# Performance work log

Measured on AMD Instinct MI355X. Metric: run time of the kernel, lower is better.

The kernel has to match this reference:

```python
import jax, jax.numpy as jnp
import numpy as np

B, S, D_MODEL, H = 2, 2048, 2048, 16
DQK = D_MODEL // H            # 128
DV = D_MODEL * 2 // H // 3    # 85 (GLU branch)
SCALE = DQK ** -0.5
ROPE_BASE = 10000.0


def apply_rope(x):
    # x: [B, S, H, D], NeoX-style half rotation
    D = x.shape[-1]
    half = D // 2
    inv_freq = 1.0 / (ROPE_BASE ** (jnp.arange(half, dtype=jnp.float32) / half))
    ang = jnp.arange(x.shape[1], dtype=jnp.float32)[:, None] * inv_freq[None, :]  # [S, half]
    cos = jnp.cos(ang)[None, :, None, :]
    sin = jnp.sin(ang)[None, :, None, :]
    x1, x2 = x[..., :half], x[..., half:]
    return jnp.concatenate([x1 * cos - x2 * sin, x2 * cos + x1 * sin], axis=-1)


def setup_inputs() -> dict:
    key = jax.random.key(0)
    ks = jax.random.split(key, 12)
    init = lambda k, shape, fan_in: jax.random.uniform(k, shape, jnp.float32, -1.0, 1.0) * (fan_in ** -0.5)
    q = jax.random.normal(ks[0], (B, S, D_MODEL), jnp.float32)
    k = jax.random.normal(ks[1], (B, S, D_MODEL), jnp.float32)
    v = jax.random.normal(ks[2], (B, S, D_MODEL), jnp.float32)
    # causal boolean mask: True = masked (upper triangle)
    mask = jnp.triu(jnp.ones((S, S), dtype=bool), k=1)
    Wq = init(ks[3], (D_MODEL, DQK * H), D_MODEL)
    bq = init(ks[4], (DQK * H,), D_MODEL)
    Wk = init(ks[5], (D_MODEL, DQK * H), D_MODEL)
    bk = init(ks[6], (DQK * H,), D_MODEL)
    Wv = init(ks[7], (D_MODEL, DV * H * 2), D_MODEL)
    bv = init(ks[8], (DV * H * 2,), D_MODEL)
    Wo = init(ks[9], (DV * H, D_MODEL), DV * H)
    bo = init(ks[10], (D_MODEL,), DV * H)
    return {"q": q, "k": k, "v": v, "mask": mask,
            "Wq": Wq, "bq": bq, "Wk": Wk, "bk": bk,
            "Wv": Wv, "bv": bv, "Wo": Wo, "bo": bo}


def reference(q, k, v, mask, Wq, bq, Wk, bk, Wv, bv, Wo, bo):
    qp = q @ Wq + bq                      # [B,S,H*DQK]
    kp = k @ Wk + bk                      # [B,S,H*DQK]
    vp = v @ Wv + bv                      # [B,S,2*H*DV]
    # GLU over the FULL last dim (matches torch chunk(2, dim=-1) before unflatten)
    half = DV * H
    vg = vp[..., :half] * jax.nn.silu(vp[..., half:])   # [B,S,H*DV]
    qh = qp.reshape(B, S, H, DQK)
    kh = kp.reshape(B, S, H, DQK)
    vh = vg.reshape(B, S, H, DV)
    qh = apply_rope(qh)
    kh = apply_rope(kh)
    # [B,H,S,D]
    qh = qh.transpose(0, 2, 1, 3)
    kh = kh.transpose(0, 2, 1, 3)
    vh = vh.transpose(0, 2, 1, 3)
    score = jnp.einsum('bhqd,bhkd->bhqk', qh, kh) * SCALE  # [B,H,S,S]
    score = jnp.where(mask[None, None, :, :], -jnp.inf, score)
    attn = jax.nn.softmax(score, axis=-1)
    o = jnp.einsum('bhqk,bhkd->bhqd', attn, vh)            # [B,H,S,DV]
    o = o.transpose(0, 2, 1, 3).reshape(B, S, H * DV)
    return o @ Wo + bo                                     # [B,S,D_MODEL]
```

## Files before the change

kernel.cpp:

```cpp
#include <hip/hip_runtime.h>
#include <cstdint>
#include <cmath>

typedef __bf16 bf16;
typedef __bf16 bf16x8 __attribute__((ext_vector_type(8)));
typedef float f32x4 __attribute__((ext_vector_type(4)));

#define B_      2
#define S_      2048
#define H_      16
#define DQK_    128
#define DV_     85
#define DVP_    96
#define DMODEL_ 2048
#define NKV_    1360
#define KH_     1536
#define NV_     2720
#define NVP_    2816
#define SCALE_  0.08838834764831845f
#define QSCALE_ 0.12752044442215615f
#define M2_     16.0f
#define L2_10K_ 13.287712379549449f

__device__ __forceinline__ void lds_cp16(const void* g, void* l) {
    __builtin_amdgcn_global_load_lds(
        (const __attribute__((address_space(1))) unsigned int*)(uintptr_t)g,
        (__attribute__((address_space(3))) unsigned int*)(uintptr_t)l,
        16, 0, 0);
}

__global__ __launch_bounds__(256) void detect_dtype(const unsigned int* __restrict__ w,
                                                    int* __restrict__ flag) {
    __shared__ int cnt;
    if (threadIdx.x == 0) cnt = 0;
    __syncthreads();
    unsigned v = w[threadIdx.x];
    unsigned e = (v >> 7) & 0xFFu;
    if (e > 100u && e < 140u) atomicAdd(&cnt, 1);
    __syncthreads();
    if (threadIdx.x == 0) *flag = (cnt >= 200) ? 1 : 0;
}

__global__ __launch_bounds__(256) void norm_mat(const void* __restrict__ src, bf16* __restrict__ dst,
                                                const int* __restrict__ flag, long n8) {
    long i = (long)blockIdx.x * 256 + threadIdx.x;
    if (i >= n8) return;
    if (*flag) {
        ((bf16x8*)dst)[i] = ((const bf16x8*)src)[i];
    } else {
        const float* s = (const float*)src;
        bf16x8 v;
#pragma unroll
        for (int j = 0; j < 8; ++j) v[j] = (bf16)s[i * 8 + j];
        ((bf16x8*)dst)[i] = v;
    }
}

__global__ __launch_bounds__(256) void norm_bias4(
    const void* __restrict__ s0, const void* __restrict__ s1,
    const void* __restrict__ s2, const void* __restrict__ s3,
    float* __restrict__ d0, float* __restrict__ d1,
    float* __restrict__ d2, float* __restrict__ d3,
    const int* __restrict__ flag) {
    int j = blockIdx.x * 256 + threadIdx.x;
    const void* s; float* d;
    if (j < DMODEL_) { s = s0; d = d0; }
    else if ((j -= DMODEL_) < DMODEL_) { s = s1; d = d1; }
    else if ((j -= DMODEL_) < NV_) { s = s2; d = d2; }
    else if ((j -= NV_) < DMODEL_) { s = s3; d = d3; }
    else return;
    d[j] = (*flag) ? (float)((const bf16*)s)[j] : ((const float*)s)[j];
}

__global__ __launch_bounds__(256) void transpose_qk_dyn(
    const void* __restrict__ inq, const void* __restrict__ ink,
    bf16* __restrict__ outq, bf16* __restrict__ outk, const int* __restrict__ flag) {
    __shared__ bf16 tile[32][33];
    const bool isbf = (*flag != 0);
    const void* in = blockIdx.z ? ink : inq;
    bf16* out = blockIdx.z ? outk : outq;
    int r0 = blockIdx.x * 32, c0 = blockIdx.y * 32;
    int tx = threadIdx.x, ty = threadIdx.y;
#pragma unroll
    for (int i = 0; i < 32; i += 8) {
        size_t idx = (size_t)(r0 + ty + i) * DMODEL_ + c0 + tx;
        tile[ty + i][tx] = isbf ? ((const bf16*)in)[idx] : (bf16)((const float*)in)[idx];
    }
    __syncthreads();
#pragma unroll
    for (int i = 0; i < 32; i += 8)
        out[(size_t)(c0 + ty + i) * DMODEL_ + r0 + tx] = tile[tx][ty + i];
}

__global__ __launch_bounds__(256) void transpose_wvi_dyn(
    const void* __restrict__ in, bf16* __restrict__ out, const int* __restrict__ flag) {
    __shared__ bf16 tile[32][34];
    const bool isbf = (*flag != 0);
    int n0 = blockIdx.x * 32, k0 = blockIdx.y * 32;
    int tx = threadIdx.x, ty = threadIdx.y;
    int fl = (n0 >> 1) + (tx & 15), vg = tx >> 4;
    int c = vg * NKV_ + fl;
    int nl = 2 * (tx & 15) + vg;
#pragma unroll
    for (int i = 0; i < 32; i += 8) {
        bf16 v = (bf16)0.0f;
        if (fl < NKV_) {
            size_t idx = (size_t)(k0 + ty + i) * NV_ + c;
            v = isbf ? ((const bf16*)in)[idx] : (bf16)((const float*)in)[idx];
        }
        tile[ty + i][nl] = v;
    }
    __syncthreads();
#pragma unroll
    for (int i = 0; i < 32; i += 8)
        out[(size_t)(n0 + ty + i) * DMODEL_ + k0 + tx] = tile[tx][ty + i];
}

__global__ __launch_bounds__(256) void transpose_wo_dyn(
    const void* __restrict__ in, bf16* __restrict__ out, const int* __restrict__ flag) {
    __shared__ bf16 tile[32][33];
    const bool isbf = (*flag != 0);
    int k0 = blockIdx.x * 32, n0 = blockIdx.y * 32;
    int tx = threadIdx.x, ty = threadIdx.y;
#pragma unroll
    for (int i = 0; i < 32; i += 8) {
        int k = k0 + ty + i, c = n0 + tx;
        int hh = k / DVP_, dd = k - hh * DVP_;
        bf16 v = (bf16)0.0f;
        if (dd < DV_) {
            size_t idx = (size_t)(hh * DV_ + dd) * DMODEL_ + c;
            v = isbf ? ((const bf16*)in)[idx] : (bf16)((const float*)in)[idx];
        }
        tile[ty + i][tx] = v;
    }
    __syncthreads();
#pragma unroll
    for (int i = 0; i < 32; i += 8) {
        int n = n0 + ty + i, k = k0 + tx;
        out[(size_t)n * KH_ + k] = tile[tx][ty + i];
    }
}

template <int NT, class AF>
__device__ __forceinline__ void gemm256_loop(
    AF aaddr, const bf16* __restrict__ Bt, int ldb, int n0,
    bf16* sA, bf16* sB, f32x4 (&acc)[8][4])
{
    const int tid = threadIdx.x, lane = tid & 63, w = tid >> 6;
    const int fm = lane & 15, quad = lane >> 4;
    const int wm = (w >> 2) * 128, wn = (w & 3) * 64;
    const int row0 = tid >> 2;
    const int kk8 = (((tid >> 3) ^ tid) & 3) * 8;
    const int qsz = (quad ^ ((fm >> 1) & 3)) * 8;

    auto stageA = [&](int u, int sl) {
        const int c = u * 32 + kk8;
        lds_cp16(aaddr(row0, c),       &sA[sl * 8192 + w * 512]);
        lds_cp16(aaddr(row0 + 128, c), &sA[sl * 8192 + 4096 + w * 512]);
    };
    auto stageB = [&](int u, int sl) {
        const int c = u * 32 + kk8;
        lds_cp16(Bt + (size_t)(n0 + row0) * ldb + c,       &sB[sl * 8192 + w * 512]);
        lds_cp16(Bt + (size_t)(n0 + row0 + 128) * ldb + c, &sB[sl * 8192 + 4096 + w * 512]);
    };

    stageA(0, 0); stageA(1, 1);
    stageB(0, 0); stageB(1, 1);
    stageA(2, 2); stageA(3, 3);
    asm volatile("s_waitcnt vmcnt(4)" ::: "memory");
    __builtin_amdgcn_sched_barrier(0);
    __builtin_amdgcn_s_barrier();
    __builtin_amdgcn_sched_barrier(0);

    for (int t = 0; t < NT; ++t) {
        const int u0 = 2 * t;
        const int tm3 = t % 3;
        const int slA0 = 2 * tm3;
        const int slB0 = 2 * (t & 1);
        const int slAs = 2 * ((t + 2) % 3);
        const int slBs = 2 * ((t + 1) & 1);
        const bf16* tA0 = sA + slA0 * 8192;
        const bf16* tA1 = tA0 + 8192;
        const bf16* tB0 = sB + slB0 * 8192;
        const bf16* tB1 = tB0 + 8192;
#pragma unroll
        for (int p = 0; p < 4; ++p) {
            const int mh = p >> 1, nh = p & 1;
            bf16x8 af[2][4], bfv[2][2];
#pragma unroll
            for (int i = 0; i < 4; ++i) {
                const int ro = (wm + mh * 64 + i * 16 + fm) * 32 + qsz;
                af[0][i] = *(const bf16x8*)&tA0[ro];
                af[1][i] = *(const bf16x8*)&tA1[ro];
            }
#pragma unroll
            for (int j = 0; j < 2; ++j) {
                const int ro = (wn + nh * 32 + j * 16 + fm) * 32 + qsz;
                bfv[0][j] = *(const bf16x8*)&tB0[ro];
                bfv[1][j] = *(const bf16x8*)&tB1[ro];
            }
            if (t + 1 < NT) {
                if      (p == 0) stageB(u0 + 2, slBs);
                else if (p == 1) stageB(u0 + 3, slBs + 1);
                else if (t + 2 < NT) {
                    if (p == 2) stageA(u0 + 4, slAs);
                    else        stageA(u0 + 5, slAs + 1);
                }
            }
            __builtin_amdgcn_sched_barrier(0);
            __builtin_amdgcn_s_barrier();
            asm volatile("s_waitcnt lgkmcnt(0)" ::: "memory");
            __builtin_amdgcn_sched_barrier(0);
            __builtin_amdgcn_s_setprio(1);
#pragma unroll
            for (int kh = 0; kh < 2; ++kh)
#pragma unroll
                for (int i = 0; i < 4; ++i)
#pragma unroll
                    for (int j = 0; j < 2; ++j)
                        acc[mh * 4 + i][nh * 2 + j] = __builtin_amdgcn_mfma_f32_16x16x32_bf16(
                            af[kh][i], bfv[kh][j], acc[mh * 4 + i][nh * 2 + j], 0, 0, 0);
            __builtin_amdgcn_s_setprio(0);
            __builtin_amdgcn_sched_barrier(0);
            if (p == 3) {
                if      (t + 2 < NT) asm volatile("s_waitcnt vmcnt(4)" ::: "memory");
                else if (t + 1 < NT) asm volatile("s_waitcnt vmcnt(0)" ::: "memory");
                __builtin_amdgcn_sched_barrier(0);
            }
            __builtin_amdgcn_s_barrier();
            __builtin_amdgcn_sched_barrier(0);
        }
    }
}

__global__ __launch_bounds__(512, 2) void gemm_qk_rope256(
    const bf16* __restrict__ Aq, const bf16* __restrict__ Ak,
    const bf16* __restrict__ Btq, const bf16* __restrict__ Btk,
    const float* __restrict__ bq, const float* __restrict__ bk,
    bf16* __restrict__ qt, bf16* __restrict__ ktp) {
    extern __shared__ char smem[];
    bf16* sA = (bf16*)smem;
    bf16* sB = (bf16*)(smem + 98304);
    const int z = blockIdx.z;
    const bf16* A     = z ? Ak  : Aq;
    const bf16* Bt    = z ? Btk : Btq;
    const float* bias = z ? bk  : bq;
    bf16* dst         = z ? ktp : qt;
    const float qs    = z ? 1.0f : QSCALE_;
    const int tid = threadIdx.x, lane = tid & 63, w = tid >> 6;
    const int fm = lane & 15, quad = lane >> 4;
    const int wm = (w >> 2) * 128, wn = (w & 3) * 64;
    const int m0 = blockIdx.x * 256, n0 = blockIdx.y * 256;
    f32x4 acc[8][4] = {};
    auto aaddr = [&](int row, int k) -> const bf16* {
        return A + (size_t)(m0 + row) * DMODEL_ + k;
    };
    gemm256_loop<32>(aaddr, Bt, DMODEL_, n0, sA, sB, acc);

    float bv[4];
#pragma unroll
    for (int jn = 0; jn < 4; ++jn) bv[jn] = bias[n0 + wn + jn * 16 + fm];
    const int b = m0 >> 11, sb = m0 & (S_ - 1);
    const int hbase = n0 >> 7;
    bf16* ep = (bf16*)smem;
    __syncthreads();
#pragma unroll
    for (int g = 0; g < 4; ++g) {
        if ((w >> 2) == (g >> 1)) {
#pragma unroll
            for (int i2 = 0; i2 < 4; ++i2) {
                const int i = (g & 1) * 4 + i2;
#pragma unroll
                for (int jn = 0; jn < 4; ++jn)
#pragma unroll
                    for (int r = 0; r < 4; ++r)
                        ep[(i2 * 16 + quad * 4 + r) * 264 + wn + jn * 16 + fm] =
                            (bf16)(acc[i][jn][r] + bv[jn]);
            }
        }
        __syncthreads();
#pragma unroll
        for (int it2 = 0; it2 < 4; ++it2) {
            int task = it2 * 512 + tid;
            int lr = task >> 5, ch = task & 31;
            int s = sb + g * 64 + lr;
            int h = hbase + (ch >> 4);
            int cl0 = (ch * 8) & 127;
            bf16x8 v  = *(const bf16x8*)&ep[lr * 264 + ch * 8];
            bf16x8 uu = *(const bf16x8*)&ep[lr * 264 + ((ch * 8) ^ 64)];
            bf16x8 o8;
#pragma unroll
            for (int j = 0; j < 8; ++j) {
                int cl = cl0 + j, dd = cl & 63;
                float ang = (float)s * exp2f(-(float)dd * (L2_10K_ / 64.0f));
                float sn, cs;
                __sincosf(ang, &sn, &cs);
                float x = (float)v[j], y = (float)uu[j];
                float ov = (cl < 64) ? (x * cs - y * sn) : (x * cs + y * sn);
                o8[j] = (bf16)(ov * qs);
            }
            *(bf16x8*)&dst[((size_t)(b * H_ + h) * S_ + s) * DQK_ + cl0] = o8;
        }
        __syncthreads();
    }
}

__global__ __launch_bounds__(512, 2) void gemm_v_swiglu256(
    const bf16* __restrict__ A, const bf16* __restrict__ Bt,
    const float* __restrict__ bias, bf16* __restrict__ vt) {
    extern __shared__ char smem[];
    bf16* sA = (bf16*)smem;
    bf16* sB = (bf16*)(smem + 98304);
    const int tid = threadIdx.x, lane = tid & 63, w = tid >> 6;
    const int fm = lane & 15, quad = lane >> 4;
    const int wm = (w >> 2) * 128, wn = (w & 3) * 64;
    const int m0 = blockIdx.x * 256, n0 = blockIdx.y * 256;
    f32x4 acc[8][4] = {};
    auto aaddr = [&](int row, int k) -> const bf16* {
        return A + (size_t)(m0 + row) * DMODEL_ + k;
    };
    gemm256_loop<32>(aaddr, Bt, DMODEL_, n0, sA, sB, acc);

    float bv[4];
#pragma unroll
    for (int jn = 0; jn < 4; ++jn) {
        int col = n0 + wn + jn * 16 + fm;
        bv[jn] = (col < NV_) ? bias[(col & 1) * NKV_ + (col >> 1)] : 0.0f;
    }
    bf16* ep2 = (bf16*)smem;
    __syncthreads();
    const bool isval = ((fm & 1) == 0);
    const int flb = (wn >> 1) + (fm >> 1);
#pragma unroll
    for (int i = 0; i < 8; ++i)
#pragma unroll
        for (int jn = 0; jn < 4; ++jn)
#pragma unroll
            for (int r = 0; r < 4; ++r) {
                float ag = acc[i][jn][r] + bv[jn];
                float part = __shfl_xor(ag, 1, 64);
                if (isval) {
                    float gg = part;
                    float out = ag * gg / (1.0f + __expf(-gg));
                    ep2[(flb + jn * 8) * 264 + wm + i * 16 + quad * 4 + r] = (bf16)out;
                }
            }
    __syncthreads();
    const int b = m0 >> 11, s0 = m0 & (S_ - 1);
#pragma unroll
    for (int it2 = 0; it2 < 8; ++it2) {
        int task = it2 * 512 + tid;
        int fl_local = task >> 5, ch = task & 31;
        int flat = blockIdx.y * 128 + fl_local;
        if (flat < NKV_) {
            int h = (flat * 1543) >> 17;
            int d = flat - h * DV_;
            bf16x8 vv = *(const bf16x8*)&ep2[fl_local * 264 + ch * 8];
            *(bf16x8*)&vt[((size_t)(b * H_ + h) * DVP_ + d) * S_ + s0 + ch * 8] = vv;
        }
    }
}

__global__ __launch_bounds__(256) void vt_pad(bf16* __restrict__ vt) {
    int idx = blockIdx.x * 256 + threadIdx.x;
    if (idx >= 32 * 11 * 2048) return;
    int s = idx & (S_ - 1);
    int rest = idx >> 11;
    int dpad = 85 + rest % 11;
    int bh = rest / 11;
    vt[((size_t)bh * DVP_ + dpad) * S_ + s] = (bf16)((dpad == 95) ? 1.0f : 0.0f);
}

__global__ __launch_bounds__(256) void gemm_bt_oh(
    const bf16* __restrict__ Oh, const bf16* __restrict__ Bt,
    const float* __restrict__ bias, bf16* __restrict__ C, float* __restrict__ Cf,
    const int* __restrict__ outflag) {
    __shared__ bf16 As[128 * 32];
    __shared__ bf16 Bs[128 * 32];
    const int t = threadIdx.x, lane = t & 63, w = t >> 6;
    const int m0 = blockIdx.x * 128, n0 = blockIdx.y * 128;
    const int wm = (w >> 1) * 64, wn = (w & 1) * 64;
    const int fm = lane & 15, quad = lane >> 4, fk = quad * 8;
    const int srow = lane >> 2, scol = (lane & 3) * 8;
    f32x4 acc[4][4] = {};
    for (int k0 = 0; k0 < KH_; k0 += 32) {
        __syncthreads();
#pragma unroll
        for (int j = 0; j < 2; ++j) {
            int c = j * 4 + w;
            int m = m0 + c * 16 + srow;
            int k = k0 + scol;
            int hh = k / DVP_, dd = k - hh * DVP_;
            const bf16* ga = Oh + ((size_t)((m >> 11) * H_ + hh) * S_ + (m & (S_ - 1))) * DVP_ + dd;
            lds_cp16(ga, &As[c * 512]);
            lds_cp16(Bt + (size_t)(n0 + c * 16 + srow) * KH_ + k0 + scol, &Bs[c * 512]);
        }
        __syncthreads();
        bf16x8 af[4], bfr[4];
#pragma unroll
        for (int i = 0; i < 4; ++i) {
            af[i]  = *(const bf16x8*)&As[(wm + i * 16 + fm) * 32 + fk];
            bfr[i] = *(const bf16x8*)&Bs[(wn + i * 16 + fm) * 32 + fk];
        }
#pragma unroll
        for (int i = 0; i < 4; ++i)
#pragma unroll
            for (int jn = 0; jn < 4; ++jn)
                acc[i][jn] = __builtin_amdgcn_mfma_f32_16x16x32_bf16(af[i], bfr[jn], acc[i][jn], 0, 0, 0);
    }
    bool bf16out = (*outflag != 0);
#pragma unroll
    for (int jn = 0; jn < 4; ++jn) {
        int col = n0 + wn + jn * 16 + fm;
        float bv = bias[col];
#pragma unroll
        for (int i = 0; i < 4; ++i) {
            int rowb = m0 + wm + i * 16 + quad * 4;
            if (bf16out) {
#pragma unroll
                for (int r = 0; r < 4; ++r)
                    C[(size_t)(rowb + r) * DMODEL_ + col] = (bf16)(acc[i][jn][r] + bv);
            } else {
#pragma unroll
                for (int r = 0; r < 4; ++r)
                    Cf[(size_t)(rowb + r) * DMODEL_ + col] = acc[i][jn][r] + bv;
            }
        }
    }
}

__global__ __launch_bounds__(256) void attn_split(
    const bf16* __restrict__ qt, const bf16* __restrict__ kt,
    const bf16* __restrict__ vt,
    bf16* __restrict__ Opart, float* __restrict__ lpart) {
    const int bh = blockIdx.x, qb = blockIdx.y, split = blockIdx.z;
    if (split * 8 > qb) return;
    __shared__ bf16 Ks[64 * 128];
    __shared__ bf16 Vs[96 * 64];
    __shared__ bf16 plds[4][16 * 72];
    const int t = threadIdx.x, lane = t & 63, w = t >> 6;
    const int fm = lane & 15, quad = lane >> 4;
    const int h = bh & 15, b = bh >> 4;
    const int q0 = qb * 64 + w * 16;
    const int g = qb >> 3;
    const int pidx = bh * 80 + 4 * g * (g + 1) + (qb & 7) * (g + 1) + split;

    const bf16* qbase = qt + ((size_t)(b * H_ + h) * S_ + q0 + fm) * DQK_ + quad * 8;
    bf16x8 aq[4];
#pragma unroll
    for (int kb = 0; kb < 4; ++kb) aq[kb] = *(const bf16x8*)(qbase + kb * 32);
    const bf16* kbase = kt + (size_t)(b * H_ + h) * S_ * DQK_;
    const bf16* vbase = vt + (size_t)(b * H_ + h) * DVP_ * S_;

    const float NEG_INF = -__builtin_inff();
    f32x4 oacc[6] = {};
    bf16* pl = &plds[w][0];

    const int t0 = split * 8;
    const int t1 = min(t0 + 8, qb + 1);
    for (int it = t0; it < t1; ++it) {
        const int k0 = it * 64;
        __syncthreads();
#pragma unroll
        for (int iw = 0; iw < 4; ++iw) {
            int flat = (w * 4 + iw) * 64 + lane;
            int r = flat >> 4, c = (flat & 15) ^ (r & 15);
            lds_cp16(kbase + (size_t)(k0 + r) * DQK_ + c * 8, &Ks[(w * 4 + iw) * 512]);
        }
#pragma unroll
        for (int iw = 0; iw < 3; ++iw) {
            int flat = (w * 3 + iw) * 64 + lane;
            int r = flat >> 3, c = (flat & 7) ^ (r & 7);
            lds_cp16(vbase + (size_t)r * S_ + k0 + c * 8, &Vs[(w * 3 + iw) * 512]);
        }
        __syncthreads();
        f32x4 sc[4] = {};
#pragma unroll
        for (int nt = 0; nt < 4; ++nt) {
            if (k0 + nt * 16 <= q0 + 15) {
                const int row16 = (nt * 16 + fm) * 16;
#pragma unroll
                for (int kb = 0; kb < 4; ++kb) {
                    const bf16* kp = &Ks[(row16 + ((kb * 4 + quad) ^ fm)) * 8];
                    sc[nt] = __builtin_amdgcn_mfma_f32_16x16x32_bf16(aq[kb], *(const bf16x8*)kp, sc[nt], 0, 0, 0);
                }
            }
        }
        if (it == qb) {
#pragma unroll
            for (int nt = 0; nt < 4; ++nt) {
                int col = k0 + nt * 16 + fm;
#pragma unroll
                for (int r = 0; r < 4; ++r) {
                    int rowq = q0 + quad * 4 + r;
                    if (col > rowq) sc[nt][r] = NEG_INF;
                }
            }
        }
#pragma unroll
        for (int nt = 0; nt < 4; ++nt)
#pragma unroll
            for (int r = 0; r < 4; ++r)
                pl[(quad * 4 + r) * 72 + nt * 16 + fm] =
                    (bf16)__builtin_amdgcn_exp2f(sc[nt][r] - M2_);
        asm volatile("s_waitcnt lgkmcnt(0)" ::: "memory");
        bf16x8 pa0 = *(const bf16x8*)(pl + fm * 72 + quad * 8);
        bf16x8 pa1 = *(const bf16x8*)(pl + fm * 72 + 32 + quad * 8);
#pragma unroll
        for (int n2 = 0; n2 < 6; ++n2) {
            int row8 = (n2 * 16 + fm) * 8;
            const bf16* v0 = &Vs[(row8 + (quad ^ (fm & 7))) * 8];
            const bf16* v1 = &Vs[(row8 + ((4 + quad) ^ (fm & 7))) * 8];
            oacc[n2] = __builtin_amdgcn_mfma_f32_16x16x32_bf16(pa0, *(const bf16x8*)v0, oacc[n2], 0, 0, 0);
            oacc[n2] = __builtin_amdgcn_mfma_f32_16x16x32_bf16(pa1, *(const bf16x8*)v1, oacc[n2], 0, 0, 0);
        }
    }
    float lv[4], inv_l[4];
#pragma unroll
    for (int r = 0; r < 4; ++r) {
        lv[r] = __shfl(oacc[5][r], (lane & 48) | 15, 64);
        inv_l[r] = (lv[r] > 0.f) ? 1.0f / lv[r] : 0.0f;
    }
    if (fm == 0) {
#pragma unroll
        for (int r = 0; r < 4; ++r) {
            int row = w * 16 + quad * 4 + r;
            lpart[(size_t)pidx * 64 + row] = lv[r];
        }
    }
#pragma unroll
    for (int n2 = 0; n2 < 6; ++n2)
#pragma unroll
        for (int r = 0; r < 4; ++r) {
            int row = w * 16 + quad * 4 + r;
            Opart[((size_t)pidx * 64 + row) * DVP_ + n2 * 16 + fm] = (bf16)(oacc[n2][r] * inv_l[r]);
        }
}

__global__ __launch_bounds__(256) void attn_combine2(
    const bf16* __restrict__ Opart, const float* __restrict__ lpart,
    bf16* __restrict__ oh) {
    const int bh = blockIdx.x, qb = blockIdx.y;
    const int g = qb >> 3, nact = g + 1;
    const int pidx0 = bh * 80 + 4 * g * (g + 1) + (qb & 7) * (g + 1);
    const int t = threadIdx.x;
#pragma unroll
    for (int i = 0; i < 3; ++i) {
        int idx = i * 256 + t;
        int row = idx / 12, ch = idx - row * 12;
        float W = 0.f, wgt[4];
        for (int p = 0; p < nact; ++p) {
            wgt[p] = lpart[(size_t)(pidx0 + p) * 64 + row];
            W += wgt[p];
        }
        float invW = (W > 0.f) ? 1.0f / W : 0.0f;
        float acc[8] = {};
        for (int p = 0; p < nact; ++p) {
            bf16x8 v = *(const bf16x8*)&Opart[((size_t)(pidx0 + p) * 64 + row) * DVP_ + ch * 8];
#pragma unroll
            for (int j = 0; j < 8; ++j) acc[j] += wgt[p] * (float)v[j];
        }
        bf16x8 o8;
#pragma unroll
        for (int j = 0; j < 8; ++j) o8[j] = (bf16)(acc[j] * invW);
        *(bf16x8*)&oh[((size_t)bh * S_ + qb * 64 + row) * DVP_ + ch * 8] = o8;
    }
}

extern "C" void kernel_launch(void* const* d_in, const int* in_sizes, int n_in,
                              void* d_out, int out_size, void* d_ws, size_t ws_size,
                              hipStream_t stream) {
    const void* qin = d_in[0];
    const void* kin = d_in[1];
    const void* vin = d_in[2];
    const void* Wq = d_in[4];
    const void* bq = d_in[5];
    const void* Wk = d_in[6];
    const void* bk = d_in[7];
    const void* Wv = d_in[8];
    const void* bv = d_in[9];
    const void* Wo = d_in[10];
    const void* bo = d_in[11];

    char* ws = (char*)d_ws;
    bf16* qt   = (bf16*)(ws);
    bf16* ktp  = (bf16*)(ws + 16777216);
    char* R1   = ws + 33554432;
    bf16* scrq = (bf16*)(R1);
    bf16* scrk = (bf16*)(R1 + 16777216);
    bf16* wTq  = (bf16*)(R1 + 33554432);
    bf16* wTk  = (bf16*)(R1 + 41943040);
    bf16* scrv = (bf16*)(R1);
    bf16* wTvi = (bf16*)(R1 + 16777216);
    bf16*  wTo   = (bf16*)(R1);
    bf16*  Opart = (bf16*)(R1 + 6291456);
    float* lpart = (float*)(R1 + 37748736);
    bf16* vtp = (bf16*)(ws + 84148224);
    bf16* oh  = (bf16*)(ws + 96731136);
    float* bqf = (float*)(ws + 109314048);
    float* bkf = bqf + DMODEL_;
    float* bvf = bkf + DMODEL_;
    float* bof = bvf + NV_;
    int*  flag = (int*)(bof + DMODEL_);

    dim3 tb(32, 8);
    auto nblk = [](long n8) { return (int)((n8 + 255) / 256); };
    long n8_x = (long)B_ * S_ * DMODEL_ / 8;

    static bool attr_done = false;
    if (!attr_done) {
        hipFuncSetAttribute((const void*)gemm_qk_rope256,
                            hipFuncAttributeMaxDynamicSharedMemorySize, 163840);
        hipFuncSetAttribute((const void*)gemm_v_swiglu256,
                            hipFuncAttributeMaxDynamicSharedMemorySize, 163840);
        attr_done = true;
    }

    detect_dtype<<<1, 256, 0, stream>>>((const unsigned int*)qin, flag);
    norm_bias4<<<(3 * DMODEL_ + NV_ + 255) / 256, 256, 0, stream>>>(
        bq, bk, bv, bo, bqf, bkf, bvf, bof, flag);
    vt_pad<<<(32 * 11 * 2048) / 256, 256, 0, stream>>>(vtp);

    norm_mat<<<nblk(n8_x), 256, 0, stream>>>(qin, scrq, flag, n8_x);
    norm_mat<<<nblk(n8_x), 256, 0, stream>>>(kin, scrk, flag, n8_x);
    transpose_qk_dyn<<<dim3(64, 64, 2), tb, 0, stream>>>(Wq, Wk, wTq, wTk, flag);
    gemm_qk_rope256<<<dim3(16, 8, 2), 512, 163840, stream>>>(
        scrq, scrk, wTq, wTk, bqf, bkf, qt, ktp);

    norm_mat<<<nblk(n8_x), 256, 0, stream>>>(vin, scrv, flag, n8_x);
    transpose_wvi_dyn<<<dim3(NVP_ / 32, DMODEL_ / 32), tb, 0, stream>>>(Wv, wTvi, flag);
    gemm_v_swiglu256<<<dim3(16, NVP_ / 256), 512, 163840, stream>>>(scrv, wTvi, bvf, vtp);

    transpose_wo_dyn<<<dim3(KH_ / 32, DMODEL_ / 32), tb, 0, stream>>>(Wo, wTo, flag);

    attn_split<<<dim3(32, 32, 4), 256, 0, stream>>>(qt, ktp, vtp, Opart, lpart);
    attn_combine2<<<dim3(32, 32), 256, 0, stream>>>(Opart, lpart, oh);

    gemm_bt_oh<<<dim3(32, 16), 256, 0, stream>>>(oh, wTo, bof, (bf16*)d_out, (float*)d_out, flag);
}
```

Before: 500.8 us.

## Restructure GEMM inner loop by k-half and cut per-phase barriers

Replaces the four quadrant phases per tile with two k-half phases. Each phase loads the full 8x4 fragment set and issues 32 MFMAs, and the workgroup barriers inside each phase are dropped, leaving a single barrier at the end of each tile. This is meant to cut s_barrier synchronisation overhead and give longer uninterrupted MFMA runs. The cost is more live fragment registers, and there is a risk of LDS write-after-read hazards: stage writes now go into slots other waves may still be reading without an intervening barrier.

```diff
diff --git a/kernel.cpp b/kernel.cpp
--- a/kernel.cpp
+++ b/kernel.cpp
@@ -174,62 +174,43 @@
 
     for (int t = 0; t < NT; ++t) {
         const int u0 = 2 * t;
-        const int tm3 = t % 3;
-        const int slA0 = 2 * tm3;
+        const int slA0 = 2 * (t % 3);
         const int slB0 = 2 * (t & 1);
         const int slAs = 2 * ((t + 2) % 3);
         const int slBs = 2 * ((t + 1) & 1);
-        const bf16* tA0 = sA + slA0 * 8192;
-        const bf16* tA1 = tA0 + 8192;
-        const bf16* tB0 = sB + slB0 * 8192;
-        const bf16* tB1 = tB0 + 8192;
-#pragma unroll
-        for (int p = 0; p < 4; ++p) {
-            const int mh = p >> 1, nh = p & 1;
-            bf16x8 af[2][4], bfv[2][2];
-#pragma unroll
-            for (int i = 0; i < 4; ++i) {
-                const int ro = (wm + mh * 64 + i * 16 + fm) * 32 + qsz;
-                af[0][i] = *(const bf16x8*)&tA0[ro];
-                af[1][i] = *(const bf16x8*)&tA1[ro];
+#pragma unroll
+        for (int kh = 0; kh < 2; ++kh) {
+            const bf16* tA = sA + (slA0 + kh) * 8192;
+            const bf16* tB = sB + (slB0 + kh) * 8192;
+            bf16x8 af[8], bfv[4];
+#pragma unroll
+            for (int i = 0; i < 8; ++i)
+                af[i] = *(const bf16x8*)&tA[(wm + i * 16 + fm) * 32 + qsz];
+#pragma unroll
+            for (int j = 0; j < 4; ++j)
+                bfv[j] = *(const bf16x8*)&tB[(wn + j * 16 + fm) * 32 + qsz];
+            if (kh == 0) {
+                if (t + 1 < NT) { stageB(u0 + 2, slBs); stageB(u0 + 3, slBs + 1); }
+            } else {
+                if (t + 2 < NT) { stageA(u0 + 4, slAs); stageA(u0 + 5, slAs + 1); }
             }
-#pragma unroll
-            for (int j = 0; j < 2; ++j) {
-                const int ro = (wn + nh * 32 + j * 16 + fm) * 32 + qsz;
-                bfv[0][j] = *(const bf16x8*)&tB0[ro];
-                bfv[1][j] = *(const bf16x8*)&tB1[ro];
-            }
-            if (t + 1 < NT) {
-                if      (p == 0) stageB(u0 + 2, slBs);
-                else if (p == 1) stageB(u0 + 3, slBs + 1);
-                else if (t + 2 < NT) {
-                    if (p == 2) stageA(u0 + 4, slAs);
-                    else        stageA(u0 + 5, slAs + 1);
-                }
-            }
-            __builtin_amdgcn_sched_barrier(0);
-            __builtin_amdgcn_s_barrier();
             asm volatile("s_waitcnt lgkmcnt(0)" ::: "memory");
             __builtin_amdgcn_sched_barrier(0);
             __builtin_amdgcn_s_setprio(1);
 #pragma unroll
-            for (int kh = 0; kh < 2; ++kh)
-#pragma unroll
-                for (int i = 0; i < 4; ++i)
-#pragma unroll
-                    for (int j = 0; j < 2; ++j)
-                        acc[mh * 4 + i][nh * 2 + j] = __builtin_amdgcn_mfma_f32_16x16x32_bf16(
-                            af[kh][i], bfv[kh][j], acc[mh * 4 + i][nh * 2 + j], 0, 0, 0);
+            for (int i = 0; i < 8; ++i)
+#pragma unroll
+                for (int j = 0; j < 4; ++j)
+                    acc[i][j] = __builtin_amdgcn_mfma_f32_16x16x32_bf16(
+                        af[i], bfv[j], acc[i][j], 0, 0, 0);
             __builtin_amdgcn_s_setprio(0);
-            __builtin_amdgcn_sched_barrier(0);
-            if (p == 3) {
-                if      (t + 2 < NT) asm volatile("s_waitcnt vmcnt(4)" ::: "memory");
-                else if (t + 1 < NT) asm volatile("s_waitcnt vmcnt(0)" ::: "memory");
-                __builtin_amdgcn_sched_barrier(0);
-            }
-            __builtin_amdgcn_s_barrier();
-            __builtin_amdgcn_sched_barrier(0);
-        }
+        }
+        __builtin_amdgcn_sched_barrier(0);
+        if      (t + 2 < NT) asm volatile("s_waitcnt vmcnt(4)" ::: "memory");
+        else if (t + 1 < NT) asm volatile("s_waitcnt vmcnt(0)" ::: "memory");
+        __builtin_amdgcn_sched_barrier(0);
+        __builtin_amdgcn_s_barrier();
+        __builtin_amdgcn_sched_barrier(0);
     }
 }
 
```

After: 469.7 us. 1.07x faster.
